# Kernel optimization log

Hardware: AMD Instinct MI355X
Metric: run time of the kernel (lower is better)

The kernel has to match this reference:

```python
import jax, jax.numpy as jnp
import numpy as np

B, N, DIM = 4, 2048, 768
HEADS, DH, DEPTH = 12, 64, 4
W = 35                     # hard-coded window size
P = DIM // 2               # window-embedding proj dim
V4 = DIM // 4              # window-embedding value dim
PB = DIM // 4              # dynamic pos-bias MLP width
FF = DIM * 4
NEG = float(np.finfo(np.float32).max)


def setup_inputs() -> dict:
    key = jax.random.key(0)
    ks = iter(jax.random.split(key, 32))
    r = lambda shape: jax.random.normal(next(ks), shape, jnp.float32) * 0.02
    return dict(
        x=jax.random.normal(next(ks), (B, N, DIM), jnp.float32),
        mask=jnp.zeros((B, N), bool),
        ln1_g=jnp.ones((DEPTH, DIM)), ln1_b=jnp.zeros((DEPTH, DIM)),
        qkv_W=r((DEPTH, DIM, 3 * HEADS * DH)),
        temp=jnp.full((DEPTH,), 15.5, jnp.float32),
        we_lin_W=r((DEPTH, DIM, P)), we_q_W=r((DEPTH, P, P)),
        we_k_W=r((DEPTH, DIM, P)), we_v_W=r((DEPTH, DIM, V4)),
        we_bos=jnp.zeros((DEPTH, V4)), we_scale=jnp.ones((DEPTH,)),
        out_W=r((DEPTH, DIM + V4, DIM)),
        ln2_g=jnp.ones((DEPTH, DIM)), ln2_b=jnp.zeros((DEPTH, DIM)),
        glu_W=r((DEPTH, DIM, 2 * FF)), glu_b=jnp.zeros((DEPTH, 2 * FF)),
        ffo_W=r((DEPTH, FF, DIM)), ffo_b=jnp.zeros((DEPTH, DIM)),
        pb_W1=r((1, PB)), pb_b1=jnp.zeros((PB,)),
        pb_W2=r((PB, PB)), pb_b2=jnp.zeros((PB,)),
        pb_W3=r((PB, HEADS)), pb_b3=jnp.zeros((HEADS,)),
    )


def _ln(x, g, b):
    m = x.mean(-1, keepdims=True)
    v = ((x - m) ** 2).mean(-1, keepdims=True)
    return (x - m) * jax.lax.rsqrt(v + 1e-5) * g + b


def _l2norm(t):
    # matches F.normalize(p=2, dim=-1): x / max(||x||, 1e-12)
    return t / jnp.maximum(jnp.linalg.norm(t, axis=-1, keepdims=True), 1e-12)


def _pos_bias(n, W1, b1, W2, b2, W3, b3):
    # DynamicPositionBias(dim=PB, depth=2): Linear->ReLU, Linear->ReLU, Linear
    pos = jnp.arange(-n + 1, n, dtype=jnp.float32)[:, None]          # (2n-1, 1)
    h = jax.nn.relu(pos @ W1 + b1)
    h = jax.nn.relu(h @ W2 + b2)
    out = h @ W3 + b3                                                # (2n-1, H)
    idx = jnp.arange(n)[:, None] - jnp.arange(n)[None, :] + n - 1    # (n, n)
    return jnp.transpose(out[idx], (2, 0, 1))                        # (H, n, n)


def _sinu(n, scale):
    # ScaledSinuEmbedding over proj dim P
    inv = 1.0 / (10000.0 ** (jnp.arange(0, P, 2, dtype=jnp.float32) / P))
    s = jnp.arange(n, dtype=jnp.float32)[:, None] * inv[None, :]
    return jnp.concatenate([jnp.sin(s), jnp.cos(s)], -1) * scale     # (n, P)


def _forward(x, mask, ln1_g, ln1_b, qkv_W, temp, we_lin_W, we_q_W, we_k_W,
             we_v_W, we_bos, we_scale, out_W, ln2_g, ln2_b, glu_W, glu_b,
             ffo_W, ffo_b, pb_W1, pb_b1, pb_W2, pb_b2, pb_W3, pb_b3):
    Bz, Nn, _ = x.shape
    pad = (-Nn) % W
    nw = (Nn + pad) // W
    bias = _pos_bias(W, pb_W1, pb_b1, pb_W2, pb_b2, pb_W3, pb_b3)    # (H, W, W)
    causal = jnp.triu(jnp.ones((W, W), bool), 1)
    mpad = jnp.concatenate([mask, jnp.ones((Bz, pad), bool)], 1).reshape(Bz, nw, W)
    valid = ~mpad                                                    # (B, w, n)
    amask = ~(valid[:, None, :, :, None] & valid[:, None, :, None, :]) | causal
    we_mask = mpad[:, :, None, :]                                    # (B, w, 1, n)
    lengths = jnp.maximum(valid.sum(-1), 1).astype(jnp.float32)[..., None, None]
    sinu35 = _sinu(W, 1.0)                                           # (W, P)

    for l in range(DEPTH):
        # ---- PreNorm + windowed cosine attention ----
        h = _ln(x, ln1_g[l], ln1_b[l])
        hp = jnp.concatenate([h, jnp.zeros((Bz, pad, DIM), h.dtype)], 1)
        hp = hp.reshape(Bz, nw, W, DIM)
        qkv = (hp @ qkv_W[l]).reshape(Bz, nw, W, HEADS, DH, 3)
        q, k, v = (jnp.transpose(qkv[..., i], (0, 3, 1, 2, 4)) for i in range(3))
        q, k = _l2norm(q), _l2norm(k)
        dots = jnp.einsum('bhwid,bhwjd->bhwij', q, k) * temp[l] + bias[None, :, None]
        dots = jnp.where(amask, -NEG, dots)
        attn = jax.nn.softmax(dots, axis=-1)
        o = jnp.einsum('bhwij,bhwjd->bhwid', attn, v)
        o = jnp.transpose(o, (0, 2, 3, 1, 4)).reshape(Bz, nw, W, HEADS * DH)
        # ---- window_embeddings: pooled prev-window embedding attention ----
        we = jnp.where(mpad[..., None], 0.0, o) @ we_lin_W[l]         # (B,w,n,P)
        we = jax.nn.relu(we.sum(-2, keepdims=True) / lengths)        # (B,w,1,P)
        wq = we @ we_q_W[l]
        k2 = o @ we_k_W[l] + sinu35 * we_scale[l]
        v2 = o @ we_v_W[l]
        d2 = jnp.einsum('bwid,bwjd->bwij', wq, k2) * (P ** -0.5)
        d2 = jnp.where(we_mask, -NEG, d2)
        o2 = jnp.einsum('bwij,bwjd->bwid', jax.nn.softmax(d2, -1), v2)  # (B,w,1,V4)
        bos = jnp.broadcast_to(we_bos[l], (Bz, 1, 1, V4))
        o2 = jnp.concatenate([bos, o2], 1)[:, :-1]                   # shift by one window
        o = jnp.concatenate([o, jnp.broadcast_to(o2, (Bz, nw, W, V4))], -1)
        o = (o @ out_W[l]).reshape(Bz, nw * W, DIM)[:, :Nn]
        x = x + o
        # ---- PreNorm + GLU feed-forward ----
        h2 = _ln(x, ln2_g[l], ln2_b[l])
        a, g = jnp.split(h2 @ glu_W[l] + glu_b[l], 2, axis=-1)
        x = x + ((a * jax.nn.silu(g)) @ ffo_W[l] + ffo_b[l])
    return x


def reference(x, mask, ln1_g, ln1_b, qkv_W, temp, we_lin_W, we_q_W, we_k_W,
              we_v_W, we_bos, we_scale, out_W, ln2_g, ln2_b, glu_W, glu_b,
              ffo_W, ffo_b, pb_W1, pb_b1, pb_W2, pb_b2, pb_W3, pb_b3):
    return _forward(x, mask, ln1_g, ln1_b, qkv_W, temp, we_lin_W, we_q_W,
                    we_k_W, we_v_W, we_bos, we_scale, out_W, ln2_g, ln2_b,
                    glu_W, glu_b, ffo_W, ffo_b, pb_W1, pb_b1, pb_W2, pb_b2,
                    pb_W3, pb_b3)
```

## Files before the change

kernel.cpp:

```cpp
#include <hip/hip_runtime.h>
#include <hip/hip_bf16.h>
#include <cstddef>
#include <cstdint>

#define B_ 4
#define N_ 2048
#define DIM_ 768
#define HEADS_ 12
#define DH_ 64
#define DEPTH_ 4
#define W_ 35
#define P_ 384
#define V4_ 192
#define FF_ 3072
#define NW_ 59
#define NPB_ (NW_*W_)
#define NTOK_ (B_*N_)
#define NWB_ (B_*NW_)
#define NTP_ (NWB_*W_)
#define NTP128_ 8320
#define NEG_ 3.402823466e+38f

typedef __bf16 bf16x8 __attribute__((ext_vector_type(8)));
typedef float  f32x4  __attribute__((ext_vector_type(4)));

#define GLOAD16(g, l) __builtin_amdgcn_global_load_lds( \
    (const __attribute__((address_space(1))) uint32_t*)(g), \
    (__attribute__((address_space(3))) uint32_t*)(l), 16, 0, 0)


__global__ __launch_bounds__(192) void posbias1_k(
    const float* __restrict__ W1, const float* __restrict__ b1,
    const float* __restrict__ W2, const float* __restrict__ b2,
    const float* __restrict__ W3, const float* __restrict__ b3,
    float* __restrict__ outk)
{
    __shared__ float h1[192];
    __shared__ float h2[192];
    int i = blockIdx.x;
    int tid = threadIdx.x;
    float pos = (float)(i - 34);
    h1[tid] = fmaxf(pos*W1[tid] + b1[tid], 0.f);
    __syncthreads();
    float s = b2[tid];
    for (int k=0;k<192;k++) s += h1[k]*W2[k*192+tid];
    h2[tid] = fmaxf(s, 0.f);
    __syncthreads();
    if (tid < 12){
        float o = b3[tid];
        for (int k=0;k<192;k++) o += h2[k]*W3[k*12+tid];
        outk[i*12+tid] = o;
    }
}

__global__ void posbias2_k(const float* __restrict__ outk, float* __restrict__ bias)
{
    int e = threadIdx.x + blockIdx.x*blockDim.x;
    if (e >= HEADS_*W_*W_) return;
    int h=e/(W_*W_); int rem=e%(W_*W_); int i=rem/W_; int j=rem%W_;
    bias[e] = outk[(i-j+W_-1)*12 + h];
}

__global__ void sinu_k(float* __restrict__ sinu)
{
    int i = blockIdx.x;
    int k = threadIdx.x;
    float inv = powf(10000.f, -(float)k/192.f);
    float s = (float)i * inv;
    sinu[i*P_ + k]       = sinf(s);
    sinu[i*P_ + 192 + k] = cosf(s);
}

__global__ void len_k(const unsigned char* __restrict__ mask, float* __restrict__ len)
{
    int bw = threadIdx.x + blockIdx.x*blockDim.x;
    if (bw >= NWB_) return;
    int b = bw / NW_, w = bw % NW_;
    int cnt = 0;
    for (int t=0;t<W_;t++){
        int g = w*W_ + t;
        if (g < N_ && mask[b*N_+g]==0) cnt++;
    }
    len[bw] = fmaxf((float)cnt, 1.f);
}

__global__ __launch_bounds__(256) void pack_k(
    const float* __restrict__ W, __bf16* __restrict__ Bp,
    int N, int Ncov, int Nld, size_t lsW, size_t lsB, int qkvperm, int ncol0)
{
    int n = blockIdx.x*256 + threadIdx.x;
    int k8 = blockIdx.y, l = blockIdx.z;
    if (n >= Ncov) return;
    bf16x8 v;
    if (n < N){
        int sn = n;
        if (qkvperm){ int s = n/768, hd = n - s*768; sn = hd*3 + s; }
        const float* w = W + lsW*l + (size_t)k8*8*N + sn;
        #pragma unroll
        for (int e=0;e<8;e++) v[e] = (__bf16)w[(size_t)e*N];
    } else {
        #pragma unroll
        for (int e=0;e<8;e++) v[e] = (__bf16)0.f;
    }
    *(bf16x8*)(Bp + lsB*l + ((size_t)k8*Nld + ncol0 + n)*8) = v;
}

__global__ __launch_bounds__(256) void ln_k(
    const float* __restrict__ x, const float* __restrict__ g,
    const float* __restrict__ b, __bf16* __restrict__ out, int padded)
{
    int r = blockIdx.x;
    int tid = threadIdx.x;
    int lane = tid & 63, wave = tid >> 6;
    int row = r; bool real = true;
    if (padded){
        int bb = r / NPB_, n = r % NPB_;
        if (n >= N_) real = false;
        row = bb*N_ + n;
    }
    float v0=0,v1=0,v2=0;
    if (real){
        const float* xr = x + (size_t)row*DIM_;
        v0 = xr[tid]; v1 = xr[tid+256]; v2 = xr[tid+512];
    }
    float s1 = v0+v1+v2;
    float s2 = v0*v0+v1*v1+v2*v2;
    #pragma unroll
    for (int off=32; off; off>>=1){
        s1 += __shfl_xor(s1, off);
        s2 += __shfl_xor(s2, off);
    }
    __shared__ float a1[4], a2[4];
    if (lane==0){ a1[wave]=s1; a2[wave]=s2; }
    __syncthreads();
    s1 = a1[0]+a1[1]+a1[2]+a1[3];
    s2 = a2[0]+a2[1]+a2[2]+a2[3];
    float m   = s1 * (1.f/768.f);
    float var = s2 * (1.f/768.f) - m*m;
    float inv = rsqrtf(var + 1e-5f);
    __bf16* o = out + (size_t)r*DIM_;
    if (!real){ o[tid]=(__bf16)0.f; o[tid+256]=(__bf16)0.f; o[tid+512]=(__bf16)0.f; return; }
    o[tid]     = (__bf16)((v0-m)*inv*g[tid]     + b[tid]);
    o[tid+256] = (__bf16)((v1-m)*inv*g[tid+256] + b[tid+256]);
    o[tid+512] = (__bf16)((v2-m)*inv*g[tid+512] + b[tid+512]);
}

template<int EPI, bool DUAL, int BM>
__global__ __launch_bounds__(256) void mgemm_k(
    const __bf16* __restrict__ A, const __bf16* __restrict__ Bp,
    float* __restrict__ Cf, __bf16* __restrict__ Cb, float* __restrict__ Cf2,
    const float* __restrict__ bias, const float* __restrict__ extra,
    const float* __restrict__ scale_ptr,
    int M, int K, int Nc, int Nld, int Cld)
{
    constexpr int NF = DUAL ? 2 : 4;
    constexpr int BN = DUAL ? 64 : 128;
    constexpr int MF = BM / 32;
    constexpr int AS = BM * 32;
    constexpr int BS = BN * 32;
    constexpr int NL = BM/64 + 2;
    __shared__ alignas(16) __bf16 As[3*AS];
    __shared__ alignas(16) __bf16 Bs[3*BS];
    __shared__ alignas(16) __bf16 Gs[DUAL ? 3*BS : 16];
    const int tid = threadIdx.x;
    const int lane = tid & 63, wave = tid >> 6;
    const int wr = wave >> 1, wc = wave & 1;
    const int m0 = blockIdx.y*BM;
    const int n0 = blockIdx.x*(BN >> (DUAL?0:0));
    const int lk = lane >> 4, lr = lane & 15;
    f32x4 acc[MF][NF] = {};
    f32x4 acc2[DUAL?MF:1][NF] = {};

    auto stage = [&](int wb, int kt){
        const int k0 = kt * 32;
        #pragma unroll
        for (int q = 0; q < BM/64; q++){
            int i = tid + q*256;
            int r = i & (BM-1), k8 = i / BM;
            GLOAD16(A + (size_t)(m0 + r)*K + k0 + k8*8, As + (size_t)(wb*AS + i*8));
        }
        if constexpr (!DUAL){
            #pragma unroll
            for (int q = 0; q < 2; q++){
                int i = tid + q*256;
                int n = i & 127, k8 = i >> 7;
                GLOAD16(Bp + ((size_t)(k0/8 + k8)*Nld + n0 + n)*8, Bs + (size_t)(wb*BS + i*8));
            }
        } else {
            const int n = tid & 63, k8 = tid >> 6;
            GLOAD16(Bp + ((size_t)(k0/8 + k8)*Nld + n0 + n)*8,       Bs + (size_t)(wb*BS + tid*8));
            GLOAD16(Bp + ((size_t)(k0/8 + k8)*Nld + n0 + n + FF_)*8, Gs + (size_t)(wb*BS + tid*8));
        }
    };

    const int nk = K >> 5;
    stage(0, 0);
    if (nk > 1) stage(1, 1);
    int rb = 0;
    for (int t = 0; t < nk; ++t){
        if (t == nk-1){
            asm volatile("s_waitcnt vmcnt(0)" ::: "memory");
        } else {
            if constexpr (NL == 3) asm volatile("s_waitcnt vmcnt(3)" ::: "memory");
            else                   asm volatile("s_waitcnt vmcnt(4)" ::: "memory");
        }
        __builtin_amdgcn_s_barrier();
        __builtin_amdgcn_sched_barrier(0);
        if (t + 2 < nk){
            int wb = rb + 2; if (wb >= 3) wb -= 3;
            stage(wb, t+2);
        }
        const __bf16* as = As + (size_t)rb*AS;
        bf16x8 af[MF];
        #pragma unroll
        for (int m=0;m<MF;m++)
            af[m] = *(const bf16x8*)(as + ((size_t)(lk*BM + wr*(BM/2) + m*16 + lr))*8);
        const __bf16* bs = Bs + (size_t)rb*BS;
        bf16x8 bfr[NF];
        #pragma unroll
        for (int n=0;n<NF;n++)
            bfr[n] = *(const bf16x8*)(bs + ((size_t)(lk*BN + wc*(BN/2) + n*16 + lr))*8);
        #pragma unroll
        for (int m=0;m<MF;m++)
            #pragma unroll
            for (int n=0;n<NF;n++)
                acc[m][n] = __builtin_amdgcn_mfma_f32_16x16x32_bf16(af[m], bfr[n], acc[m][n], 0,0,0);
        if constexpr (DUAL){
            const __bf16* gs = Gs + (size_t)rb*BS;
            bf16x8 gfr[NF];
            #pragma unroll
            for (int n=0;n<NF;n++)
                gfr[n] = *(const bf16x8*)(gs + ((size_t)(lk*BN + wc*(BN/2) + n*16 + lr))*8);
            #pragma unroll
            for (int m=0;m<MF;m++)
                #pragma unroll
                for (int n=0;n<NF;n++)
                    acc2[m][n] = __builtin_amdgcn_mfma_f32_16x16x32_bf16(af[m], gfr[n], acc2[m][n], 0,0,0);
        }
        rb++; if (rb >= 3) rb = 0;
    }

    const int lq = lane >> 4;
    #pragma unroll
    for (int m=0;m<MF;m++){
        #pragma unroll
        for (int r=0;r<4;r++){
            int row = m0 + wr*(BM/2) + m*16 + lq*4 + r;
            if (row >= M) continue;
            int urow = 0, bwrow = 0;
            if (EPI==5){
                int bb = row / NPB_, n = row % NPB_;
                if (n >= N_) continue;
                urow = bb*N_ + n;
                bwrow = bb*NW_ + n/W_;
            }
            #pragma unroll
            for (int n=0;n<NF;n++){
                int col = n0 + wc*(BN/2) + n*16 + lr;
                if (col >= Nc) continue;
                float v = acc[m][n][r];
                if (EPI==1){
                    Cb[(size_t)row*Cld + col] = (__bf16)v;
                } else if (EPI==3){
                    Cf[(size_t)row*Cld + col] += v + bias[col];
                } else if (EPI==4){
                    float a_ = v + bias[col];
                    float g_ = acc2[m][n][r] + bias[col + FF_];
                    Cb[(size_t)row*Cld + col] = (__bf16)(a_ * (g_ / (1.f + expf(-g_))));
                } else if (EPI==5){
                    Cf[(size_t)urow*DIM_ + col] += v + extra[(size_t)bwrow*DIM_ + col];
                } else if (EPI==7){
                    if (col < P_){
                        int tt = (row % NPB_) % W_;
                        Cf[(size_t)row*P_ + col] = v + extra[tt*P_ + col]*scale_ptr[0];
                    } else {
                        Cf2[(size_t)row*V4_ + (col - P_)] = v;
                    }
                }
            }
        }
    }
}

__global__ __launch_bounds__(256) void gemm0_k(
    const float* __restrict__ A, const float* __restrict__ Bw,
    float* __restrict__ C, int M, int K, int Nc, int ldb)
{
    __shared__ float As[16][65];
    __shared__ float Bs[16][65];
    const int m0 = blockIdx.y*64, n0 = blockIdx.x*64;
    const int tid = threadIdx.x;
    const int ty = tid>>4, tx = tid&15;
    float acc[4][4] = {};
    for (int k0=0; k0<K; k0+=16){
        #pragma unroll
        for (int i=0;i<4;i++){
            int e = tid + i*256;
            int m = e>>4, kk = e&15;
            int mg = m0+m;
            As[kk][m] = (mg < M) ? A[(size_t)mg*K + k0+kk] : 0.f;
        }
        #pragma unroll
        for (int i=0;i<4;i++){
            int e = tid + i*256;
            int kk = e>>6, n = e&63;
            Bs[kk][n] = Bw[(size_t)(k0+kk)*ldb + n0+n];
        }
        __syncthreads();
        #pragma unroll
        for (int kk=0;kk<16;kk++){
            float a[4], bv[4];
            #pragma unroll
            for (int i=0;i<4;i++) a[i] = As[kk][ty*4+i];
            #pragma unroll
            for (int j=0;j<4;j++) bv[j] = Bs[kk][tx*4+j];
            #pragma unroll
            for (int i=0;i<4;i++)
                #pragma unroll
                for (int j=0;j<4;j++) acc[i][j] += a[i]*bv[j];
        }
        __syncthreads();
    }
    #pragma unroll
    for (int i=0;i<4;i++){
        int mg = m0 + ty*4 + i;
        if (mg >= M) continue;
        #pragma unroll
        for (int j=0;j<4;j++){
            int c = n0 + tx*4 + j;
            if (c >= Nc) continue;
            C[(size_t)mg*Nc + c] = acc[i][j];
        }
    }
}

__global__ __launch_bounds__(256) void attn_k(
    const __bf16* __restrict__ qkv, const unsigned char* __restrict__ mask,
    const float* __restrict__ bias, const float* __restrict__ temp_p,
    __bf16* __restrict__ obuf, float* __restrict__ osum)
{
    int bid = blockIdx.x;
    int w = bid % NW_;
    int h = (bid / NW_) % HEADS_;
    int b = bid / (NW_*HEADS_);
    int tid = threadIdx.x;
    __shared__ float qs[W_*DH_], ks[W_*DH_], vs[W_*DH_];
    __shared__ float sc[W_*W_];
    __shared__ float osacc[4][64];
    __shared__ int vf[W_];
    int bw = b*NW_ + w;
    int rbase = bw*W_;
    for (int e=tid; e<W_*DH_; e+=256){
        int t=e>>6, d=e&63;
        size_t idx = (size_t)(rbase+t)*(3*DIM_) + h*DH_ + d;
        qs[e]=(float)qkv[idx];
        ks[e]=(float)qkv[idx+768];
        vs[e]=(float)qkv[idx+1536];
    }
    if (tid < W_){
        int g = w*W_ + tid;
        vf[tid] = (g < N_) && (mask[b*N_+g]==0);
    }
    __syncthreads();
    for (int e=tid; e<2*W_; e+=256){
        float* src = (e<W_)? qs : ks;
        int t = (e<W_)? e : e-W_;
        float s=0;
        for (int d=0;d<DH_;d++){ float v=src[t*DH_+d]; s+=v*v; }
        float inv = 1.f / fmaxf(sqrtf(s), 1e-12f);
        for (int d=0;d<DH_;d++) src[t*DH_+d] *= inv;
    }
    __syncthreads();
    float temp = temp_p[0];
    for (int e=tid; e<W_*W_; e+=256){
        int i=e/W_, j=e%W_;
        float s;
        if (!vf[i] || !vf[j] || j>i) s = -NEG_;
        else {
            float acc=0;
            for (int d=0;d<DH_;d++) acc += qs[i*DH_+d]*ks[j*DH_+d];
            s = acc*temp + bias[(h*W_+i)*W_+j];
        }
        sc[e]=s;
    }
    __syncthreads();
    if (tid < W_){
        int i=tid;
        float mx=-INFINITY;
        for (int j=0;j<W_;j++) mx=fmaxf(mx, sc[i*W_+j]);
        float sum=0;
        for (int j=0;j<W_;j++){ float e_=expf(sc[i*W_+j]-mx); sc[i*W_+j]=e_; sum+=e_; }
        float inv=1.f/sum;
        for (int j=0;j<W_;j++) sc[i*W_+j]*=inv;
    }
    __syncthreads();
    int wavei = tid >> 6, d = tid & 63;
    float psum = 0.f;
    for (int i = wavei; i < W_; i += 4){
        float s=0;
        for (int j=0;j<W_;j++) s += sc[i*W_+j]*vs[j*DH_+d];
        obuf[(size_t)(rbase+i)*DIM_ + h*DH_ + d] = (__bf16)s;
        if (vf[i]) psum += s;
    }
    osacc[wavei][d] = psum;
    __syncthreads();
    if (tid < 64)
        osum[(size_t)bw*DIM_ + h*DH_ + tid] =
            osacc[0][tid]+osacc[1][tid]+osacc[2][tid]+osacc[3][tid];
}

__global__ __launch_bounds__(384) void wefuse_k(
    const float* __restrict__ osum, const float* __restrict__ we_lin,
    const float* __restrict__ we_q, const float* __restrict__ k2,
    const float* __restrict__ v2, const unsigned char* __restrict__ mask,
    const float* __restrict__ len, float* __restrict__ o2)
{
    int bw = blockIdx.x;
    int b = bw / NW_, w = bw % NW_;
    int tid = threadIdx.x;
    __shared__ float osr[768], werr[384], wqr[384], pp[W_];
    osr[tid]     = osum[(size_t)bw*DIM_ + tid];
    osr[tid+384] = osum[(size_t)bw*DIM_ + tid + 384];
    __syncthreads();
    float invlen = 1.f / len[bw];
    float s = 0;
    for (int k=0;k<768;k++) s += osr[k]*we_lin[(size_t)k*P_ + tid];
    werr[tid] = fmaxf(s*invlen, 0.f);
    __syncthreads();
    s = 0;
    for (int k=0;k<384;k++) s += werr[k]*we_q[(size_t)k*P_ + tid];
    wqr[tid] = s;
    __syncthreads();
    if (tid < W_){
        int g = w*W_ + tid;
        bool val = (g < N_) && (mask[b*N_+g]==0);
        float sv = -NEG_;
        if (val){
            float acc=0;
            const float* kr = k2 + (size_t)(bw*W_+tid)*P_;
            for (int c=0;c<P_;c++) acc += wqr[c]*kr[c];
            sv = acc * 0.05103103630798287f;
        }
        pp[tid]=sv;
    }
    __syncthreads();
    if (tid==0){
        float mx=-INFINITY;
        for (int j=0;j<W_;j++) mx=fmaxf(mx,pp[j]);
        float sum=0;
        for (int j=0;j<W_;j++){ float e=expf(pp[j]-mx); pp[j]=e; sum+=e; }
        float inv=1.f/sum;
        for (int j=0;j<W_;j++) pp[j]*=inv;
    }
    __syncthreads();
    if (tid < V4_){
        float sv=0;
        for (int j=0;j<W_;j++) sv += pp[j]*v2[(size_t)(bw*W_+j)*V4_ + tid];
        o2[(size_t)bw*V4_ + tid] = sv;
    }
}

__global__ void o2shift_k(const float* __restrict__ o2, const float* __restrict__ bos,
                          float* __restrict__ o2u)
{
    int e = threadIdx.x + blockIdx.x*blockDim.x;
    if (e >= NWB_*V4_) return;
    int bw = e / V4_, c = e % V4_;
    int w = bw % NW_;
    o2u[e] = (w==0) ? bos[c] : o2[e - V4_];
}


extern "C" void kernel_launch(void* const* d_in, const int* in_sizes, int n_in,
                              void* d_out, int out_size, void* d_ws, size_t ws_size,
                              hipStream_t stream)
{
    const float* x       = (const float*)d_in[0];
    const unsigned char* mask = (const unsigned char*)d_in[1];
    const float* ln1_g   = (const float*)d_in[2];
    const float* ln1_b   = (const float*)d_in[3];
    const float* qkv_W   = (const float*)d_in[4];
    const float* temp    = (const float*)d_in[5];
    const float* we_lin_W= (const float*)d_in[6];
    const float* we_q_W  = (const float*)d_in[7];
    const float* we_k_W  = (const float*)d_in[8];
    const float* we_v_W  = (const float*)d_in[9];
    const float* we_bos  = (const float*)d_in[10];
    const float* we_scale= (const float*)d_in[11];
    const float* out_W   = (const float*)d_in[12];
    const float* ln2_g   = (const float*)d_in[13];
    const float* ln2_b   = (const float*)d_in[14];
    const float* glu_W   = (const float*)d_in[15];
    const float* glu_b   = (const float*)d_in[16];
    const float* ffo_W   = (const float*)d_in[17];
    const float* ffo_b   = (const float*)d_in[18];
    const float* pb_W1   = (const float*)d_in[19];
    const float* pb_b1   = (const float*)d_in[20];
    const float* pb_W2   = (const float*)d_in[21];
    const float* pb_b2   = (const float*)d_in[22];
    const float* pb_W3   = (const float*)d_in[23];
    const float* pb_b3   = (const float*)d_in[24];

    float* xc = (float*)d_out;

    char* p = (char*)d_ws;
    auto alloc = [&](size_t bytes)->char* {
        char* r = p; p += (bytes + 255) & ~(size_t)255; return r;
    };
    float* f_outk = (float*)alloc((size_t)69*12*4);
    float* f_bias = (float*)alloc((size_t)HEADS_*W_*W_*4);
    float* f_sinu = (float*)alloc((size_t)W_*P_*4);
    float* f_len  = (float*)alloc((size_t)NWB_*4);
    float* f_osum = (float*)alloc((size_t)NWB_*DIM_*4);
    float* f_o2   = (float*)alloc((size_t)NWB_*V4_*4);
    float* f_o2u  = (float*)alloc((size_t)NWB_*V4_*4);
    float* f_o2p  = (float*)alloc((size_t)NWB_*DIM_*4);
    __bf16* w_qkv = (__bf16*)alloc((size_t)DEPTH_*96*2304*8*2);
    __bf16* w_kv  = (__bf16*)alloc((size_t)DEPTH_*96*640*8*2);
    __bf16* w_out = (__bf16*)alloc((size_t)DEPTH_*96*768*8*2);
    __bf16* w_glu = (__bf16*)alloc((size_t)DEPTH_*96*6144*8*2);
    __bf16* w_ffo = (__bf16*)alloc((size_t)DEPTH_*384*768*8*2);
    char* arena = p;
    __bf16* f_hpad = (__bf16*)alloc((size_t)NTP128_*DIM_*2);
    __bf16* f_qkvb = (__bf16*)alloc((size_t)NTP_*3*DIM_*2);
    __bf16* f_obuf = (__bf16*)alloc((size_t)NTP128_*DIM_*2);
    float*  f_k2   = (float*)alloc((size_t)NTP_*P_*4);
    float*  f_v2   = (float*)alloc((size_t)NTP_*V4_*4);
    __bf16* f_h2 = (__bf16*)arena;
    __bf16* f_ag = (__bf16*)(arena + (((size_t)NTOK_*DIM_*2 + 255) & ~(size_t)255));
    (void)ws_size; (void)in_sizes; (void)n_in; (void)out_size;

    hipMemcpyAsync(xc, x, (size_t)NTOK_*DIM_*sizeof(float),
                   hipMemcpyDeviceToDevice, stream);
    posbias1_k<<<69,192,0,stream>>>(pb_W1,pb_b1,pb_W2,pb_b2,pb_W3,pb_b3,f_outk);
    posbias2_k<<<(HEADS_*W_*W_+255)/256,256,0,stream>>>(f_outk, f_bias);
    sinu_k<<<W_,192,0,stream>>>(f_sinu);
    len_k<<<1,256,0,stream>>>(mask, f_len);
    pack_k<<<dim3(9,96,DEPTH_),256,0,stream>>>(qkv_W, w_qkv, 2304, 2304, 2304,
        (size_t)768*2304, (size_t)96*2304*8, 1, 0);
    pack_k<<<dim3(2,96,DEPTH_),256,0,stream>>>(we_k_W, w_kv, 384, 384, 640,
        (size_t)768*384, (size_t)96*640*8, 0, 0);
    pack_k<<<dim3(1,96,DEPTH_),256,0,stream>>>(we_v_W, w_kv, 192, 256, 640,
        (size_t)768*192, (size_t)96*640*8, 0, 384);
    pack_k<<<dim3(3,96,DEPTH_),256,0,stream>>>(out_W, w_out, 768, 768, 768,
        (size_t)960*768, (size_t)96*768*8, 0, 0);
    pack_k<<<dim3(24,96,DEPTH_),256,0,stream>>>(glu_W, w_glu, 6144, 6144, 6144,
        (size_t)768*6144, (size_t)96*6144*8, 0, 0);
    pack_k<<<dim3(3,384,DEPTH_),256,0,stream>>>(ffo_W, w_ffo, 768, 768, 768,
        (size_t)3072*768, (size_t)384*768*8, 0, 0);

    for (int l=0;l<DEPTH_;l++){
        ln_k<<<NTP_,256,0,stream>>>(xc, ln1_g+l*DIM_, ln1_b+l*DIM_, f_hpad, 1);
        mgemm_k<1,false,128><<<dim3(18,65),256,0,stream>>>(f_hpad,
            w_qkv + (size_t)l*96*2304*8, nullptr, f_qkvb, nullptr,
            nullptr, nullptr, nullptr, NTP_, DIM_, 3*DIM_, 3*DIM_, 3*DIM_);
        attn_k<<<B_*HEADS_*NW_,256,0,stream>>>(f_qkvb, mask, f_bias, temp+l,
            f_obuf, f_osum);
        mgemm_k<7,false,64><<<dim3(5,130),256,0,stream>>>(f_obuf,
            w_kv + (size_t)l*96*640*8, f_k2, nullptr, f_v2,
            nullptr, f_sinu, we_scale+l, NTP_, DIM_, 576, 640, 0);
        wefuse_k<<<NWB_,384,0,stream>>>(f_osum, we_lin_W + (size_t)l*DIM_*P_,
            we_q_W + (size_t)l*P_*P_, f_k2, f_v2, mask, f_len, f_o2);
        o2shift_k<<<(NWB_*V4_+255)/256,256,0,stream>>>(f_o2, we_bos+l*V4_, f_o2u);
        gemm0_k<<<dim3(12,4),256,0,stream>>>(f_o2u,
            out_W + (size_t)l*(DIM_+V4_)*DIM_ + (size_t)DIM_*DIM_,
            f_o2p, NWB_, V4_, DIM_, DIM_);
        mgemm_k<5,false,64><<<dim3(6,130),256,0,stream>>>(f_obuf,
            w_out + (size_t)l*96*768*8, xc, nullptr, nullptr,
            nullptr, f_o2p, nullptr, NTP_, DIM_, DIM_, DIM_, DIM_);

        ln_k<<<NTOK_,256,0,stream>>>(xc, ln2_g+l*DIM_, ln2_b+l*DIM_, f_h2, 0);
        mgemm_k<4,true,128><<<dim3(48,64),256,0,stream>>>(f_h2,
            w_glu + (size_t)l*96*6144*8, nullptr, f_ag, nullptr,
            glu_b + (size_t)l*2*FF_, nullptr, nullptr,
            NTOK_, DIM_, FF_, 2*FF_, FF_);
        mgemm_k<3,false,64><<<dim3(6,128),256,0,stream>>>(f_ag,
            w_ffo + (size_t)l*384*768*8, xc, nullptr, nullptr,
            ffo_b + (size_t)l*DIM_, nullptr, nullptr,
            NTOK_, FF_, DIM_, DIM_, DIM_);
    }
}
```

Before: 2.217 ms.

## Fuse out-projection into window-KV GEMM and defer window bias to LN2/FFO

Packs the out-projection weights next to the window-embedding k/v weights so one GEMM over the attention output produces k2, v2 and the residual update to x. The per-window o2 projection term is no longer added in a separate pass: LN2 adds it on the fly and the FFO epilogue adds it into the residual. This removes one GEMM launch and one re-read of the attention output. The GLU dual GEMM also moves to 512-thread blocks with 256-row tiles, so each block reuses its weight tile across more rows. The larger tiles and the extra pass over the fused GEMM's columns change occupancy and register pressure.

```diff
diff --git a/kernel.cpp b/kernel.cpp
--- a/kernel.cpp
+++ b/kernel.cpp
@@ -18,7 +18,7 @@
 #define NTOK_ (B_*N_)
 #define NWB_ (B_*NW_)
 #define NTP_ (NWB_*W_)
-#define NTP128_ 8320
+#define NTPA_ 8448
 #define NEG_ 3.402823466e+38f
 
 typedef __bf16 bf16x8 __attribute__((ext_vector_type(8)));
@@ -107,7 +107,8 @@
 
 __global__ __launch_bounds__(256) void ln_k(
     const float* __restrict__ x, const float* __restrict__ g,
-    const float* __restrict__ b, __bf16* __restrict__ out, int padded)
+    const float* __restrict__ b, __bf16* __restrict__ out,
+    const float* __restrict__ o2p, int padded)
 {
     int r = blockIdx.x;
     int tid = threadIdx.x;
@@ -122,6 +123,11 @@
     if (real){
         const float* xr = x + (size_t)row*DIM_;
         v0 = xr[tid]; v1 = xr[tid+256]; v2 = xr[tid+512];
+        if (o2p){
+            int bb = row / N_, nn = row % N_;
+            const float* op = o2p + (size_t)(bb*NW_ + nn/W_)*DIM_;
+            v0 += op[tid]; v1 += op[tid+256]; v2 += op[tid+512];
+        }
     }
     float s1 = v0+v1+v2;
     float s2 = v0*v0+v1*v1+v2*v2;
@@ -145,20 +151,22 @@
     o[tid+512] = (__bf16)((v2-m)*inv*g[tid+512] + b[tid+512]);
 }
 
-template<int EPI, bool DUAL, int BM>
-__global__ __launch_bounds__(256) void mgemm_k(
+template<int EPI, bool DUAL, int BM, int NT>
+__global__ __launch_bounds__(NT) void mgemm_k(
     const __bf16* __restrict__ A, const __bf16* __restrict__ Bp,
     float* __restrict__ Cf, __bf16* __restrict__ Cb, float* __restrict__ Cf2,
+    float* __restrict__ Cx,
     const float* __restrict__ bias, const float* __restrict__ extra,
     const float* __restrict__ scale_ptr,
     int M, int K, int Nc, int Nld, int Cld)
 {
-    constexpr int NF = DUAL ? 2 : 4;
     constexpr int BN = DUAL ? 64 : 128;
-    constexpr int MF = BM / 32;
+    constexpr int WM = NT / 128;
+    constexpr int RS = BM / WM;
+    constexpr int MF = RS / 16;
+    constexpr int NF = (BN/2) / 16;
     constexpr int AS = BM * 32;
     constexpr int BS = BN * 32;
-    constexpr int NL = BM/64 + 2;
     __shared__ alignas(16) __bf16 As[3*AS];
     __shared__ alignas(16) __bf16 Bs[3*BS];
     __shared__ alignas(16) __bf16 Gs[DUAL ? 3*BS : 16];
@@ -166,7 +174,7 @@
     const int lane = tid & 63, wave = tid >> 6;
     const int wr = wave >> 1, wc = wave & 1;
     const int m0 = blockIdx.y*BM;
-    const int n0 = blockIdx.x*(BN >> (DUAL?0:0));
+    const int n0 = blockIdx.x*BN;
     const int lk = lane >> 4, lr = lane & 15;
     f32x4 acc[MF][NF] = {};
     f32x4 acc2[DUAL?MF:1][NF] = {};
@@ -174,18 +182,24 @@
     auto stage = [&](int wb, int kt){
         const int k0 = kt * 32;
         #pragma unroll
-        for (int q = 0; q < BM/64; q++){
-            int i = tid + q*256;
+        for (int q = 0; q < (BM*4)/NT; q++){
+            int i = tid + q*NT;
             int r = i & (BM-1), k8 = i / BM;
             GLOAD16(A + (size_t)(m0 + r)*K + k0 + k8*8, As + (size_t)(wb*AS + i*8));
         }
         if constexpr (!DUAL){
             #pragma unroll
-            for (int q = 0; q < 2; q++){
-                int i = tid + q*256;
+            for (int q = 0; q < 512/NT; q++){
+                int i = tid + q*NT;
                 int n = i & 127, k8 = i >> 7;
                 GLOAD16(Bp + ((size_t)(k0/8 + k8)*Nld + n0 + n)*8, Bs + (size_t)(wb*BS + i*8));
             }
+        } else if constexpr (NT == 512){
+            int i = tid & 255;
+            int n = i & 63, k8 = i >> 6;
+            size_t goff = ((size_t)(k0/8 + k8)*Nld + n0 + n + (tid < 256 ? 0 : FF_))*8;
+            __bf16* dst = (tid < 256 ? Bs : Gs) + (size_t)(wb*BS + i*8);
+            GLOAD16(Bp + goff, dst);
         } else {
             const int n = tid & 63, k8 = tid >> 6;
             GLOAD16(Bp + ((size_t)(k0/8 + k8)*Nld + n0 + n)*8,       Bs + (size_t)(wb*BS + tid*8));
@@ -198,12 +212,8 @@
     if (nk > 1) stage(1, 1);
     int rb = 0;
     for (int t = 0; t < nk; ++t){
-        if (t == nk-1){
-            asm volatile("s_waitcnt vmcnt(0)" ::: "memory");
-        } else {
-            if constexpr (NL == 3) asm volatile("s_waitcnt vmcnt(3)" ::: "memory");
-            else                   asm volatile("s_waitcnt vmcnt(4)" ::: "memory");
-        }
+        if (t == nk-1) asm volatile("s_waitcnt vmcnt(0)" ::: "memory");
+        else           asm volatile("s_waitcnt vmcnt(3)" ::: "memory");
         __builtin_amdgcn_s_barrier();
         __builtin_amdgcn_sched_barrier(0);
         if (t + 2 < nk){
@@ -214,7 +224,7 @@
         bf16x8 af[MF];
         #pragma unroll
         for (int m=0;m<MF;m++)
-            af[m] = *(const bf16x8*)(as + ((size_t)(lk*BM + wr*(BM/2) + m*16 + lr))*8);
+            af[m] = *(const bf16x8*)(as + ((size_t)(lk*BM + wr*RS + m*16 + lr))*8);
         const __bf16* bs = Bs + (size_t)rb*BS;
         bf16x8 bfr[NF];
         #pragma unroll
@@ -245,15 +255,8 @@
     for (int m=0;m<MF;m++){
         #pragma unroll
         for (int r=0;r<4;r++){
-            int row = m0 + wr*(BM/2) + m*16 + lq*4 + r;
+            int row = m0 + wr*RS + m*16 + lq*4 + r;
             if (row >= M) continue;
-            int urow = 0, bwrow = 0;
-            if (EPI==5){
-                int bb = row / NPB_, n = row % NPB_;
-                if (n >= N_) continue;
-                urow = bb*N_ + n;
-                bwrow = bb*NW_ + n/W_;
-            }
             #pragma unroll
             for (int n=0;n<NF;n++){
                 int col = n0 + wc*(BN/2) + n*16 + lr;
@@ -262,19 +265,24 @@
                 if (EPI==1){
                     Cb[(size_t)row*Cld + col] = (__bf16)v;
                 } else if (EPI==3){
-                    Cf[(size_t)row*Cld + col] += v + bias[col];
+                    int bb = row / N_, nn = row % N_;
+                    int bw = bb*NW_ + nn/W_;
+                    Cf[(size_t)row*Cld + col] += v + bias[col]
+                        + extra[(size_t)bw*DIM_ + col];
                 } else if (EPI==4){
                     float a_ = v + bias[col];
                     float g_ = acc2[m][n][r] + bias[col + FF_];
                     Cb[(size_t)row*Cld + col] = (__bf16)(a_ * (g_ / (1.f + expf(-g_))));
-                } else if (EPI==5){
-                    Cf[(size_t)urow*DIM_ + col] += v + extra[(size_t)bwrow*DIM_ + col];
-                } else if (EPI==7){
+                } else if (EPI==8){
                     if (col < P_){
                         int tt = (row % NPB_) % W_;
                         Cf[(size_t)row*P_ + col] = v + extra[tt*P_ + col]*scale_ptr[0];
+                    } else if (col < 576){
+                        Cf2[(size_t)row*V4_ + (col - P_)] = v;
                     } else {
-                        Cf2[(size_t)row*V4_ + (col - P_)] = v;
+                        int bb = row / NPB_, nn = row % NPB_;
+                        if (nn < N_)
+                            Cx[(size_t)(bb*N_ + nn)*DIM_ + (col - 576)] += v;
                     }
                 }
             }
@@ -516,14 +524,13 @@
     float* f_o2u  = (float*)alloc((size_t)NWB_*V4_*4);
     float* f_o2p  = (float*)alloc((size_t)NWB_*DIM_*4);
     __bf16* w_qkv = (__bf16*)alloc((size_t)DEPTH_*96*2304*8*2);
-    __bf16* w_kv  = (__bf16*)alloc((size_t)DEPTH_*96*640*8*2);
-    __bf16* w_out = (__bf16*)alloc((size_t)DEPTH_*96*768*8*2);
+    __bf16* w_kvo = (__bf16*)alloc((size_t)DEPTH_*96*1408*8*2);
     __bf16* w_glu = (__bf16*)alloc((size_t)DEPTH_*96*6144*8*2);
     __bf16* w_ffo = (__bf16*)alloc((size_t)DEPTH_*384*768*8*2);
     char* arena = p;
-    __bf16* f_hpad = (__bf16*)alloc((size_t)NTP128_*DIM_*2);
+    __bf16* f_hpad = (__bf16*)alloc((size_t)NTPA_*DIM_*2);
     __bf16* f_qkvb = (__bf16*)alloc((size_t)NTP_*3*DIM_*2);
-    __bf16* f_obuf = (__bf16*)alloc((size_t)NTP128_*DIM_*2);
+    __bf16* f_obuf = (__bf16*)alloc((size_t)NTPA_*DIM_*2);
     float*  f_k2   = (float*)alloc((size_t)NTP_*P_*4);
     float*  f_v2   = (float*)alloc((size_t)NTP_*V4_*4);
     __bf16* f_h2 = (__bf16*)arena;
@@ -538,45 +545,44 @@
     len_k<<<1,256,0,stream>>>(mask, f_len);
     pack_k<<<dim3(9,96,DEPTH_),256,0,stream>>>(qkv_W, w_qkv, 2304, 2304, 2304,
         (size_t)768*2304, (size_t)96*2304*8, 1, 0);
-    pack_k<<<dim3(2,96,DEPTH_),256,0,stream>>>(we_k_W, w_kv, 384, 384, 640,
-        (size_t)768*384, (size_t)96*640*8, 0, 0);
-    pack_k<<<dim3(1,96,DEPTH_),256,0,stream>>>(we_v_W, w_kv, 192, 256, 640,
-        (size_t)768*192, (size_t)96*640*8, 0, 384);
-    pack_k<<<dim3(3,96,DEPTH_),256,0,stream>>>(out_W, w_out, 768, 768, 768,
-        (size_t)960*768, (size_t)96*768*8, 0, 0);
+    pack_k<<<dim3(2,96,DEPTH_),256,0,stream>>>(we_k_W, w_kvo, 384, 384, 1408,
+        (size_t)768*384, (size_t)96*1408*8, 0, 0);
+    pack_k<<<dim3(1,96,DEPTH_),256,0,stream>>>(we_v_W, w_kvo, 192, 192, 1408,
+        (size_t)768*192, (size_t)96*1408*8, 0, 384);
+    pack_k<<<dim3(4,96,DEPTH_),256,0,stream>>>(out_W, w_kvo, 768, 832, 1408,
+        (size_t)960*768, (size_t)96*1408*8, 0, 576);
     pack_k<<<dim3(24,96,DEPTH_),256,0,stream>>>(glu_W, w_glu, 6144, 6144, 6144,
         (size_t)768*6144, (size_t)96*6144*8, 0, 0);
     pack_k<<<dim3(3,384,DEPTH_),256,0,stream>>>(ffo_W, w_ffo, 768, 768, 768,
         (size_t)3072*768, (size_t)384*768*8, 0, 0);
 
     for (int l=0;l<DEPTH_;l++){
-        ln_k<<<NTP_,256,0,stream>>>(xc, ln1_g+l*DIM_, ln1_b+l*DIM_, f_hpad, 1);
-        mgemm_k<1,false,128><<<dim3(18,65),256,0,stream>>>(f_hpad,
-            w_qkv + (size_t)l*96*2304*8, nullptr, f_qkvb, nullptr,
+        ln_k<<<NTP_,256,0,stream>>>(xc, ln1_g+l*DIM_, ln1_b+l*DIM_, f_hpad,
+            nullptr, 1);
+        mgemm_k<1,false,128,256><<<dim3(18,65),256,0,stream>>>(f_hpad,
+            w_qkv + (size_t)l*96*2304*8, nullptr, f_qkvb, nullptr, nullptr,
             nullptr, nullptr, nullptr, NTP_, DIM_, 3*DIM_, 3*DIM_, 3*DIM_);
         attn_k<<<B_*HEADS_*NW_,256,0,stream>>>(f_qkvb, mask, f_bias, temp+l,
             f_obuf, f_osum);
-        mgemm_k<7,false,64><<<dim3(5,130),256,0,stream>>>(f_obuf,
-            w_kv + (size_t)l*96*640*8, f_k2, nullptr, f_v2,
-            nullptr, f_sinu, we_scale+l, NTP_, DIM_, 576, 640, 0);
+        mgemm_k<8,false,64,256><<<dim3(11,130),256,0,stream>>>(f_obuf,
+            w_kvo + (size_t)l*96*1408*8, f_k2, nullptr, f_v2, xc,
+            nullptr, f_sinu, we_scale+l, NTP_, DIM_, 1344, 1408, 0);
         wefuse_k<<<NWB_,384,0,stream>>>(f_osum, we_lin_W + (size_t)l*DIM_*P_,
             we_q_W + (size_t)l*P_*P_, f_k2, f_v2, mask, f_len, f_o2);
         o2shift_k<<<(NWB_*V4_+255)/256,256,0,stream>>>(f_o2, we_bos+l*V4_, f_o2u);
         gemm0_k<<<dim3(12,4),256,0,stream>>>(f_o2u,
             out_W + (size_t)l*(DIM_+V4_)*DIM_ + (size_t)DIM_*DIM_,
             f_o2p, NWB_, V4_, DIM_, DIM_);
-        mgemm_k<5,false,64><<<dim3(6,130),256,0,stream>>>(f_obuf,
-            w_out + (size_t)l*96*768*8, xc, nullptr, nullptr,
-            nullptr, f_o2p, nullptr, NTP_, DIM_, DIM_, DIM_, DIM_);
-
-        ln_k<<<NTOK_,256,0,stream>>>(xc, ln2_g+l*DIM_, ln2_b+l*DIM_, f_h2, 0);
-        mgemm_k<4,true,128><<<dim3(48,64),256,0,stream>>>(f_h2,
-            w_glu + (size_t)l*96*6144*8, nullptr, f_ag, nullptr,
+
+        ln_k<<<NTOK_,256,0,stream>>>(xc, ln2_g+l*DIM_, ln2_b+l*DIM_, f_h2,
+            f_o2p, 0);
+        mgemm_k<4,true,256,512><<<dim3(48,32),512,0,stream>>>(f_h2,
+            w_glu + (size_t)l*96*6144*8, nullptr, f_ag, nullptr, nullptr,
             glu_b + (size_t)l*2*FF_, nullptr, nullptr,
             NTOK_, DIM_, FF_, 2*FF_, FF_);
-        mgemm_k<3,false,64><<<dim3(6,128),256,0,stream>>>(f_ag,
-            w_ffo + (size_t)l*384*768*8, xc, nullptr, nullptr,
-            ffo_b + (size_t)l*DIM_, nullptr, nullptr,
+        mgemm_k<3,false,64,256><<<dim3(6,128),256,0,stream>>>(f_ag,
+            w_ffo + (size_t)l*384*768*8, xc, nullptr, nullptr, nullptr,
+            ffo_b + (size_t)l*DIM_, f_o2p, nullptr,
             NTOK_, FF_, DIM_, DIM_, DIM_);
     }
 }
```

Measured after the change: 2.283 ms. +3.0%, slower.
